# Kernel optimization log

Measured on AMD Instinct MI355X. Metric: run time of the kernel, lower is better.

The kernel has to match this reference:

```python
import jax, jax.numpy as jnp
import numpy as np

B, T, DIM, H = 4, 2048, 512, 8
DECAY = 0.9

def setup_inputs():
    key = jax.random.key(0)
    ks = jax.random.split(key, 8)
    s = 1.0 / np.sqrt(DIM)
    def lin(k):
        return jax.random.normal(k, (DIM, DIM), jnp.float32) * s
    return {
        "q": jax.random.normal(ks[0], (B, T, DIM), jnp.float32),
        "k": jax.random.normal(ks[1], (B, T, DIM), jnp.float32),
        "v": jax.random.normal(ks[2], (B, T, DIM), jnp.float32),
        "Wa": lin(ks[3]), "ba": jnp.zeros((DIM,), jnp.float32),
        "Wb": lin(ks[4]), "bb": jnp.zeros((DIM,), jnp.float32),
        "Wg": lin(ks[5]), "bg": jnp.zeros((DIM,), jnp.float32),
        "Wo": lin(ks[6]), "bo": jnp.zeros((DIM,), jnp.float32),
    }

def _linear_scan(a, b):
    # h_t = a_t * h_{t-1} + b_t along time axis=1, via associative scan
    def combine(c1, c2):
        a1, b1 = c1
        a2, b2 = c2
        return a1 * a2, a2 * b1 + b2
    return jax.lax.associative_scan(combine, (a, b), axis=1)[1]

def reference(q, k, v, Wa, ba, Wb, bb, Wg, bg, Wo, bo):
    # --- Mamba-style selective scan on q (no residual) ---
    a = jax.nn.sigmoid(q @ Wa + ba)   # input-dependent decay [B,T,D]
    b = q @ Wb + bb                   # input injection       [B,T,D]
    h = _linear_scan(a, b)            # recurrent state       [B,T,D]
    g = jax.nn.sigmoid(q @ Wg + bg)   # gate
    m_out = (h * g) @ Wo + bo         # [B,T,D]

    # --- RetNet-style decay-weighted linear retention ---
    Dh = DIM // H
    qh = q.reshape(B, T, H, Dh)
    kh = k.reshape(B, T, H, Dh)
    vh = v.reshape(B, T, H, Dh)
    t = jnp.arange(T)
    delta = t[:, None] - t[None, :]           # t - s
    mask = delta >= 0                         # causal
    decay_mat = jnp.where(
        mask,
        jnp.exp(jnp.where(mask, delta, 0).astype(jnp.float32) * np.float32(np.log(DECAY))),
        0.0,
    )                                          # [T,T]
    scores = jnp.einsum('bthd,bshd->bhts', qh, kh) * decay_mat  # [B,H,T,T]
    r_out = jnp.einsum('bhts,bshd->bthd', scores, vh).reshape(B, T, DIM)

    return m_out + r_out
```

## Files before the change

### kernel.cpp

```cpp
#include <hip/hip_runtime.h>
#include <hip/hip_bf16.h>

typedef unsigned short u16;

#define BB 4
#define TT 2048
#define DIM 512
#define NH 8
#define DH 64
#define DECAY 0.9f

#define CC 64
#define NC 32
#define BHN 32

#define CHS 32
#define NSC 64

#define TM 128
#define TN 128
#define BK 64

#define SS 72

typedef __attribute__((ext_vector_type(8))) short bf16x8;
typedef __attribute__((ext_vector_type(4))) float f32x4;

__device__ __forceinline__ u16 f2bfu(float f) {
  union { float f; unsigned int u; } c; c.f = f;
  unsigned int u = c.u + 0x7FFFu + ((c.u >> 16) & 1u);
  return (u16)(u >> 16);
}
__device__ __forceinline__ float bf2f(u16 u) {
  union { unsigned int u; float f; } c; c.u = ((unsigned int)u) << 16;
  return c.f;
}

__device__ __forceinline__ void gl_lds16(const void* g, void* l) {
  __builtin_amdgcn_global_load_lds(
      (const __attribute__((address_space(1))) void*)g,
      (__attribute__((address_space(3))) void*)(unsigned int)(unsigned long long)l,
      16, 0, 0);
}

__device__ __forceinline__ void gemm_tile(
    int nTile, int mTile, const u16* __restrict__ A, const u16* __restrict__ Bt,
    const float* __restrict__ b0, const float* __restrict__ b1,
    const float* __restrict__ b2,
    void* __restrict__ C0, void* __restrict__ C1, void* __restrict__ C2,
    int act_mask, int bf16_mask, const u16* __restrict__ Radd,
    u16* As, u16* Bs, int tid) {
  int wave = tid >> 6, lane = tid & 63;
  int group = (nTile * TN) >> 9;
  const float* bias = (group == 0) ? b0 : (group == 1) ? b1 : b2;
  void* C = (group == 0) ? C0 : (group == 1) ? C1 : C2;
  int act = (act_mask >> group) & 1;
  int isbf = (bf16_mask >> group) & 1;

  int wm = (wave >> 1) * 64, wn = (wave & 1) * 64;
  int rowA = lane & 15, khalf = lane >> 4;

  f32x4 acc[4][4];
#pragma unroll
  for (int i = 0; i < 4; ++i)
#pragma unroll
    for (int j = 0; j < 4; ++j) acc[i][j] = (f32x4){0.f, 0.f, 0.f, 0.f};

  const u16* Abase = A + (size_t)mTile * TM * 512;
  const u16* Bbase = Bt + (size_t)nTile * TN * 512;

  for (int kk = 0; kk < 512; kk += BK) {
#pragma unroll
    for (int i = 0; i < 4; ++i) {
      int o = (wave * 4 + i) * 64 + lane;
      int row = o >> 3, gk = (o & 7) ^ (row & 7);
      gl_lds16(Abase + (size_t)row * 512 + kk + gk * 8, &As[o * 8]);
    }
#pragma unroll
    for (int i = 0; i < 4; ++i) {
      int o = (wave * 4 + i) * 64 + lane;
      int row = o >> 3, gk = (o & 7) ^ (row & 7);
      gl_lds16(Bbase + (size_t)row * 512 + kk + gk * 8, &Bs[o * 8]);
    }
    __syncthreads();
#pragma unroll
    for (int k0 = 0; k0 < 2; ++k0) {
      bf16x8 af[4], bfr[4];
#pragma unroll
      for (int mi = 0; mi < 4; ++mi) {
        int rr = wm + mi * 16 + rowA;
        int gk = k0 * 4 + khalf;
        int o = rr * 8 + (gk ^ (rr & 7));
        af[mi] = *(const bf16x8*)&As[o * 8];
      }
#pragma unroll
      for (int ni = 0; ni < 4; ++ni) {
        int rr = wn + ni * 16 + rowA;
        int gk = k0 * 4 + khalf;
        int o = rr * 8 + (gk ^ (rr & 7));
        bfr[ni] = *(const bf16x8*)&Bs[o * 8];
      }
#pragma unroll
      for (int mi = 0; mi < 4; ++mi)
#pragma unroll
        for (int ni = 0; ni < 4; ++ni)
          acc[mi][ni] = __builtin_amdgcn_mfma_f32_16x16x32_bf16(
              af[mi], bfr[ni], acc[mi][ni], 0, 0, 0);
    }
    __syncthreads();
  }
  int cloc = lane & 15, rq = (lane >> 4) * 4;
#pragma unroll
  for (int mi = 0; mi < 4; ++mi) {
#pragma unroll
    for (int r = 0; r < 4; ++r) {
      int m = mTile * TM + wm + mi * 16 + rq + r;
#pragma unroll
      for (int ni = 0; ni < 4; ++ni) {
        int n = (nTile * TN + wn + ni * 16 + cloc) & 511;
        float vv = acc[mi][ni][r] + bias[n];
        if (act) vv = 1.0f / (1.0f + __expf(-vv));
        if (Radd) vv += bf2f(Radd[(size_t)m * 512 + n]);
        if (isbf) ((u16*)C)[(size_t)m * 512 + n] = f2bfu(vv);
        else ((float*)C)[(size_t)m * 512 + n] = vv;
      }
    }
  }
}

__global__ __launch_bounds__(256) void k1_prep(
    const float* __restrict__ q, u16* __restrict__ qbf,
    const float* __restrict__ W0, const float* __restrict__ W1,
    const float* __restrict__ W2, const float* __restrict__ W3,
    u16* __restrict__ Wt) {
  __shared__ float t[32][33];
  int bx = blockIdx.x, tid = threadIdx.x;
  if (bx < 1024) {
    int m = bx >> 8, rem = bx & 255;
    int n0 = (rem & 15) * 32, k0 = (rem >> 4) * 32;
    const float* W = (m == 0) ? W0 : (m == 1) ? W1 : (m == 2) ? W2 : W3;
    int tx = tid & 31, ty = tid >> 5;
#pragma unroll
    for (int r = 0; r < 32; r += 8)
      t[ty + r][tx] = W[(size_t)(k0 + ty + r) * DIM + n0 + tx];
    __syncthreads();
    u16* o = Wt + (size_t)m * DIM * DIM;
#pragma unroll
    for (int r = 0; r < 32; r += 8)
      o[(size_t)(n0 + ty + r) * DIM + k0 + tx] = f2bfu(t[tx][ty + r]);
  } else {
    int i = (bx - 1024) * 256 + tid;
    float4 f = ((const float4*)q)[i];
    ushort4 u;
    u.x = f2bfu(f.x); u.y = f2bfu(f.y); u.z = f2bfu(f.z); u.w = f2bfu(f.w);
    ((ushort4*)qbf)[i] = u;
  }
}

__global__ __launch_bounds__(256) void k2_gemm1_retkv(
    const u16* __restrict__ qbf, const u16* __restrict__ WtAll,
    const float* __restrict__ ba, const float* __restrict__ bb,
    const float* __restrict__ bg,
    float* __restrict__ Abuf, u16* __restrict__ Bb16, u16* __restrict__ Gb16,
    const float* __restrict__ k, const float* __restrict__ v,
    u16* __restrict__ KVTb, u16* __restrict__ VTg) {
  __shared__ __align__(16) u16 smem[TM * BK + TN * BK];
  int bx = blockIdx.x, tid = threadIdx.x;
  if (bx < 768) {
    gemm_tile(bx % 12, bx / 12, qbf, WtAll, ba, bb, bg, Abuf, Bb16, Gb16,
              0b101, 0b110, nullptr, smem, smem + TM * BK, tid);
    return;
  }
  int idx = bx - 768;
  int bh = idx & 31, c = idx >> 5;
  int b = bh >> 3, h = bh & 7;
  int wave = tid >> 6, lane = tid & 63;
  u16* VT = smem;
  u16* KT = smem + 64 * SS;
  size_t base = ((size_t)(b * TT + c * CC)) * DIM + h * DH;
  int row = tid >> 2, part = tid & 3, e0 = part * 16;
  float w = __powf(DECAY, (float)(63 - row));
  {
    const float4* vs = (const float4*)(v + base + (size_t)row * DIM + e0);
    const float4* ks = (const float4*)(k + base + (size_t)row * DIM + e0);
#pragma unroll
    for (int u4 = 0; u4 < 4; ++u4) {
      float4 fv = vs[u4], fk = ks[u4];
      VT[(e0 + u4 * 4 + 0) * SS + row] = f2bfu(fv.x);
      VT[(e0 + u4 * 4 + 1) * SS + row] = f2bfu(fv.y);
      VT[(e0 + u4 * 4 + 2) * SS + row] = f2bfu(fv.z);
      VT[(e0 + u4 * 4 + 3) * SS + row] = f2bfu(fv.w);
      KT[(e0 + u4 * 4 + 0) * SS + row] = f2bfu(fk.x * w);
      KT[(e0 + u4 * 4 + 1) * SS + row] = f2bfu(fk.y * w);
      KT[(e0 + u4 * 4 + 2) * SS + row] = f2bfu(fk.z * w);
      KT[(e0 + u4 * 4 + 3) * SS + row] = f2bfu(fk.w * w);
    }
  }
  __syncthreads();
  {
    int e = row;
    u16* dst = VTg + ((size_t)bh * 64 + e) * TT + c * 64 + part * 16;
    *(uint4*)dst = *(const uint4*)&VT[e * SS + part * 16];
    *(uint4*)(dst + 8) = *(const uint4*)&VT[e * SS + part * 16 + 8];
  }
  int wm = (wave >> 1) * 32, wn = (wave & 1) * 32;
  int rowA = lane & 15, khalf = lane >> 4;
  f32x4 acc[2][2];
#pragma unroll
  for (int i = 0; i < 2; ++i)
#pragma unroll
    for (int j = 0; j < 2; ++j) acc[i][j] = (f32x4){0.f, 0.f, 0.f, 0.f};
#pragma unroll
  for (int k0 = 0; k0 < 2; ++k0) {
    int gk = k0 * 4 + khalf;
    bf16x8 af[2], bfr[2];
#pragma unroll
    for (int mi = 0; mi < 2; ++mi)
      af[mi] = *(const bf16x8*)&VT[(wm + mi * 16 + rowA) * SS + gk * 8];
#pragma unroll
    for (int ni = 0; ni < 2; ++ni)
      bfr[ni] = *(const bf16x8*)&KT[(wn + ni * 16 + rowA) * SS + gk * 8];
#pragma unroll
    for (int mi = 0; mi < 2; ++mi)
#pragma unroll
      for (int ni = 0; ni < 2; ++ni)
        acc[mi][ni] = __builtin_amdgcn_mfma_f32_16x16x32_bf16(
            af[mi], bfr[ni], acc[mi][ni], 0, 0, 0);
  }
  int cloc = lane & 15, rq = (lane >> 4) * 4;
  u16* o = KVTb + ((size_t)(c * BHN + bh)) * 4096;
#pragma unroll
  for (int mi = 0; mi < 2; ++mi)
#pragma unroll
    for (int r = 0; r < 4; ++r) {
      int e = wm + mi * 16 + rq + r;
#pragma unroll
      for (int ni = 0; ni < 2; ++ni)
        o[e * 64 + (wn + ni * 16 + cloc)] = f2bfu(acc[mi][ni][r]);
    }
}

__global__ __launch_bounds__(256) void k3_part_retscan(
    const float* __restrict__ a, const u16* __restrict__ bb16,
    float* __restrict__ SA, float* __restrict__ SB,
    const u16* __restrict__ KVTb, u16* __restrict__ Ptb) {
  int bx = blockIdx.x, tid = threadIdx.x;
  if (bx < 512) {
    int ci = bx >> 3, grp = bx & 7;
    int ch = grp * 256 + tid;
    int bb = ch >> 9, d = ch & 511;
    size_t base = ((size_t)bb * TT + ci * CHS) * DIM + d;
    float h = 0.f, pA = 1.f;
#pragma unroll
    for (int t = 0; t < CHS; ++t) {
      float av = a[base + (size_t)t * DIM];
      float bv = bf2f(bb16[base + (size_t)t * DIM]);
      h = fmaf(av, h, bv);
      pA *= av;
    }
    SA[ci * 2048 + ch] = pA;
    SB[ci * 2048 + ch] = h;
  } else {
    int gid = (bx - 512) * 256 + tid;
    int bh = gid >> 12, ed = gid & 4095;
    float carry = 0.f;
    const float dC = __powf(DECAY, (float)CC);
    for (int c = 0; c < NC; ++c) {
      size_t idx = ((size_t)(c * BHN + bh)) * 4096 + ed;
      Ptb[idx] = f2bfu(carry);
      carry = fmaf(dC, carry, bf2f(KVTb[idx]));
    }
  }
}

__global__ __launch_bounds__(256) void k4_apply_retout(
    const float* __restrict__ a, const u16* __restrict__ bb16,
    const u16* __restrict__ g, const float* __restrict__ SA,
    const float* __restrict__ SB, u16* __restrict__ hg,
    const u16* __restrict__ qbf, const float* __restrict__ kg,
    const u16* __restrict__ VTg, const u16* __restrict__ Ptb,
    u16* __restrict__ routb) {
  __shared__ __align__(16) u16 Sa[64 * SS];
  __shared__ float dp[66];
  int bx = blockIdx.x, tid = threadIdx.x;
  if (bx < 512) {
    int ci = bx >> 3, grp = bx & 7;
    int ch = grp * 256 + tid;
    int bb = ch >> 9, d = ch & 511;
    float carry = 0.f;
    for (int p = 0; p < ci; ++p)
      carry = fmaf(SA[p * 2048 + ch], carry, SB[p * 2048 + ch]);
    size_t base = ((size_t)bb * TT + ci * CHS) * DIM + d;
    float h = carry;
#pragma unroll
    for (int t = 0; t < CHS; ++t) {
      size_t idx = base + (size_t)t * DIM;
      h = fmaf(a[idx], h, bf2f(bb16[idx]));
      hg[idx] = f2bfu(h * bf2f(g[idx]));
    }
    return;
  }
  int idx2 = bx - 512;
  int bh = idx2 & 31, c = idx2 >> 5;
  int b = bh >> 3, h = bh & 7;
  int wave = tid >> 6, lane = tid & 63;
  size_t base = ((size_t)(b * TT + c * CC)) * DIM + h * DH;
  if (tid < 66) dp[tid] = __powf(DECAY, (float)tid);

  int wm = (wave >> 1) * 32, wn = (wave & 1) * 32;
  int rowA = lane & 15, khalf = lane >> 4;

  bf16x8 afq[2][2];
#pragma unroll
  for (int k0 = 0; k0 < 2; ++k0)
#pragma unroll
    for (int mi = 0; mi < 2; ++mi)
      afq[k0][mi] = *(const bf16x8*)(qbf + base +
          (size_t)(wm + mi * 16 + rowA) * 512 + (k0 * 4 + khalf) * 8);
  bf16x8 bfk[2][2];
#pragma unroll
  for (int k0 = 0; k0 < 2; ++k0)
#pragma unroll
    for (int ni = 0; ni < 2; ++ni) {
      const float* kp = kg + base + (size_t)(wn + ni * 16 + rowA) * 512 +
                        (k0 * 4 + khalf) * 8;
      float4 f0 = *(const float4*)kp;
      float4 f1 = *(const float4*)(kp + 4);
      bf16x8 t;
      t[0] = (short)f2bfu(f0.x); t[1] = (short)f2bfu(f0.y);
      t[2] = (short)f2bfu(f0.z); t[3] = (short)f2bfu(f0.w);
      t[4] = (short)f2bfu(f1.x); t[5] = (short)f2bfu(f1.y);
      t[6] = (short)f2bfu(f1.z); t[7] = (short)f2bfu(f1.w);
      bfk[k0][ni] = t;
    }

  f32x4 accS[2][2];
#pragma unroll
  for (int i = 0; i < 2; ++i)
#pragma unroll
    for (int j = 0; j < 2; ++j) accS[i][j] = (f32x4){0.f, 0.f, 0.f, 0.f};
#pragma unroll
  for (int k0 = 0; k0 < 2; ++k0)
#pragma unroll
    for (int mi = 0; mi < 2; ++mi)
#pragma unroll
      for (int ni = 0; ni < 2; ++ni)
        accS[mi][ni] = __builtin_amdgcn_mfma_f32_16x16x32_bf16(
            afq[k0][mi], bfk[k0][ni], accS[mi][ni], 0, 0, 0);
  __syncthreads();

  int cloc = lane & 15, rq = (lane >> 4) * 4;
#pragma unroll
  for (int mi = 0; mi < 2; ++mi)
#pragma unroll
    for (int ni = 0; ni < 2; ++ni)
#pragma unroll
      for (int r = 0; r < 4; ++r) {
        int i = wm + mi * 16 + rq + r;
        int j = wn + ni * 16 + cloc;
        float sv = (j <= i) ? accS[mi][ni][r] * dp[i - j] : 0.f;
        Sa[i * SS + j] = f2bfu(sv);
      }
#pragma unroll
  for (int mi = 0; mi < 2; ++mi) {
    float s = dp[wm + mi * 16 + rowA + 1];
#pragma unroll
    for (int k0 = 0; k0 < 2; ++k0) {
      bf16x8 t = afq[k0][mi];
#pragma unroll
      for (int u = 0; u < 8; ++u)
        t[u] = (short)f2bfu(bf2f((u16)t[u]) * s);
      afq[k0][mi] = t;
    }
  }
  __syncthreads();

  f32x4 accO[2][2];
#pragma unroll
  for (int i = 0; i < 2; ++i)
#pragma unroll
    for (int j = 0; j < 2; ++j) accO[i][j] = (f32x4){0.f, 0.f, 0.f, 0.f};
#pragma unroll
  for (int k0 = 0; k0 < 4; ++k0) {
    bf16x8 af[2], bfv[2];
#pragma unroll
    for (int mi = 0; mi < 2; ++mi) {
      if (k0 < 2)
        af[mi] = *(const bf16x8*)&Sa[(wm + mi * 16 + rowA) * SS +
                                     (k0 * 4 + khalf) * 8];
      else
        af[mi] = afq[k0 - 2][mi];
    }
#pragma unroll
    for (int ni = 0; ni < 2; ++ni) {
      int e = wn + ni * 16 + rowA;
      if (k0 < 2)
        bfv[ni] = *(const bf16x8*)(VTg + ((size_t)bh * 64 + e) * TT + c * 64 +
                                   (k0 * 4 + khalf) * 8);
      else
        bfv[ni] = *(const bf16x8*)(Ptb + ((size_t)(c * BHN + bh)) * 4096 +
                                   e * 64 + ((k0 - 2) * 4 + khalf) * 8);
    }
#pragma unroll
    for (int mi = 0; mi < 2; ++mi)
#pragma unroll
      for (int ni = 0; ni < 2; ++ni)
        accO[mi][ni] = __builtin_amdgcn_mfma_f32_16x16x32_bf16(
            af[mi], bfv[ni], accO[mi][ni], 0, 0, 0);
  }
#pragma unroll
  for (int mi = 0; mi < 2; ++mi)
#pragma unroll
    for (int r = 0; r < 4; ++r) {
      int i = wm + mi * 16 + rq + r;
#pragma unroll
      for (int ni = 0; ni < 2; ++ni) {
        int e = wn + ni * 16 + cloc;
        routb[base + (size_t)i * 512 + e] = f2bfu(accO[mi][ni][r]);
      }
    }
}

__global__ __launch_bounds__(256) void k5_gemm2(
    const u16* __restrict__ hgbf, const u16* __restrict__ Wto,
    const float* __restrict__ bo, float* __restrict__ out,
    const u16* __restrict__ routb) {
  __shared__ __align__(16) u16 smem[TM * BK + TN * BK];
  gemm_tile(blockIdx.x, blockIdx.y, hgbf, Wto, bo, bo, bo, out, out, out,
            0, 0, routb, smem, smem + TM * BK, threadIdx.x);
}

extern "C" void kernel_launch(void* const* d_in, const int* in_sizes, int n_in,
                              void* d_out, int out_size, void* d_ws, size_t ws_size,
                              hipStream_t stream) {
  const float* q  = (const float*)d_in[0];
  const float* k  = (const float*)d_in[1];
  const float* v  = (const float*)d_in[2];
  const float* Wa = (const float*)d_in[3];
  const float* ba = (const float*)d_in[4];
  const float* Wb = (const float*)d_in[5];
  const float* bb = (const float*)d_in[6];
  const float* Wg = (const float*)d_in[7];
  const float* bg = (const float*)d_in[8];
  const float* Wo = (const float*)d_in[9];
  const float* bo = (const float*)d_in[10];
  float* out = (float*)d_out;
  float* ws = (float*)d_ws;

  const size_t NEL = (size_t)BB * TT * DIM;
  float* Abuf = ws;
  float* SA = ws + NEL;
  float* SB = SA + NSC * 2048;
  u16* up = (u16*)(SB + NSC * 2048);
  u16* Bb16  = up;  up += NEL;
  u16* Gb16  = up;  up += NEL;
  u16* qbf   = up;  up += NEL;
  u16* hgbf  = up;  up += NEL;
  u16* WtAll = up;  up += 4 * DIM * DIM;
  u16* KVTb  = up;  up += (size_t)NC * BHN * 4096;
  u16* Ptb   = up;  up += (size_t)NC * BHN * 4096;
  u16* VTg   = up;  up += (size_t)BHN * 64 * TT;
  u16* routb = up;  up += NEL;

  k1_prep<<<5120, 256, 0, stream>>>(q, qbf, Wa, Wb, Wg, Wo, WtAll);

  k2_gemm1_retkv<<<1792, 256, 0, stream>>>(qbf, WtAll, ba, bb, bg,
                                           Abuf, Bb16, Gb16, k, v, KVTb, VTg);

  k3_part_retscan<<<1024, 256, 0, stream>>>(Abuf, Bb16, SA, SB, KVTb, Ptb);

  k4_apply_retout<<<1536, 256, 0, stream>>>(Abuf, Bb16, Gb16, SA, SB, hgbf,
                                            qbf, k, VTg, Ptb, routb);

  k5_gemm2<<<dim3(4, 64), 256, 0, stream>>>(hgbf, WtAll + 3 * DIM * DIM,
                                            bo, out, routb);
}
```

Before: 198.0 us.

## Rebalance GEMM work across kernels, store decay in bf16, use 128x64 tiles

The gate projection GEMM tiles move from the first GEMM kernel into the partial-scan kernel, so they run alongside the scan and retention carry work instead of lengthening the first kernel. The sigmoid decay buffer is now stored in bf16 instead of fp32, which halves its write and read traffic across three kernels. The output GEMM switches to a 128x64 tile, giving 512 blocks instead of 256 to better fill the CUs. Storing the decay in bf16 reduces the precision of the recurrence factor, which may raise error over long scans.

```diff
diff --git a/kernel.cpp b/kernel.cpp
--- a/kernel.cpp
+++ b/kernel.cpp
@@ -47,15 +47,13 @@
     int nTile, int mTile, const u16* __restrict__ A, const u16* __restrict__ Bt,
     const float* __restrict__ b0, const float* __restrict__ b1,
     const float* __restrict__ b2,
-    void* __restrict__ C0, void* __restrict__ C1, void* __restrict__ C2,
-    int act_mask, int bf16_mask, const u16* __restrict__ Radd,
-    u16* As, u16* Bs, int tid) {
+    u16* __restrict__ C0, u16* __restrict__ C1, u16* __restrict__ C2,
+    int act_mask, u16* As, u16* Bs, int tid) {
   int wave = tid >> 6, lane = tid & 63;
   int group = (nTile * TN) >> 9;
   const float* bias = (group == 0) ? b0 : (group == 1) ? b1 : b2;
-  void* C = (group == 0) ? C0 : (group == 1) ? C1 : C2;
+  u16* C = (group == 0) ? C0 : (group == 1) ? C1 : C2;
   int act = (act_mask >> group) & 1;
-  int isbf = (bf16_mask >> group) & 1;
 
   int wm = (wave >> 1) * 64, wn = (wave & 1) * 64;
   int rowA = lane & 15, khalf = lane >> 4;
@@ -120,9 +118,80 @@
         int n = (nTile * TN + wn + ni * 16 + cloc) & 511;
         float vv = acc[mi][ni][r] + bias[n];
         if (act) vv = 1.0f / (1.0f + __expf(-vv));
-        if (Radd) vv += bf2f(Radd[(size_t)m * 512 + n]);
-        if (isbf) ((u16*)C)[(size_t)m * 512 + n] = f2bfu(vv);
-        else ((float*)C)[(size_t)m * 512 + n] = vv;
+        C[(size_t)m * 512 + n] = f2bfu(vv);
+      }
+    }
+  }
+}
+
+__device__ __forceinline__ void gemm_tile64(
+    int nTile, int mTile, const u16* __restrict__ A, const u16* __restrict__ Bt,
+    const float* __restrict__ bias, float* __restrict__ C,
+    const u16* __restrict__ Radd, u16* As, u16* Bs, int tid) {
+  int wave = tid >> 6, lane = tid & 63;
+  int wm = wave * 32;
+  int rowA = lane & 15, khalf = lane >> 4;
+
+  f32x4 acc[2][4];
+#pragma unroll
+  for (int i = 0; i < 2; ++i)
+#pragma unroll
+    for (int j = 0; j < 4; ++j) acc[i][j] = (f32x4){0.f, 0.f, 0.f, 0.f};
+
+  const u16* Abase = A + (size_t)mTile * TM * 512;
+  const u16* Bbase = Bt + (size_t)nTile * 64 * 512;
+
+  for (int kk = 0; kk < 512; kk += BK) {
+#pragma unroll
+    for (int i = 0; i < 4; ++i) {
+      int o = (wave * 4 + i) * 64 + lane;
+      int row = o >> 3, gk = (o & 7) ^ (row & 7);
+      gl_lds16(Abase + (size_t)row * 512 + kk + gk * 8, &As[o * 8]);
+    }
+#pragma unroll
+    for (int i = 0; i < 2; ++i) {
+      int o = (wave * 2 + i) * 64 + lane;
+      int row = o >> 3, gk = (o & 7) ^ (row & 7);
+      gl_lds16(Bbase + (size_t)row * 512 + kk + gk * 8, &Bs[o * 8]);
+    }
+    __syncthreads();
+#pragma unroll
+    for (int k0 = 0; k0 < 2; ++k0) {
+      bf16x8 af[2], bfr[4];
+#pragma unroll
+      for (int mi = 0; mi < 2; ++mi) {
+        int rr = wm + mi * 16 + rowA;
+        int gk = k0 * 4 + khalf;
+        int o = rr * 8 + (gk ^ (rr & 7));
+        af[mi] = *(const bf16x8*)&As[o * 8];
+      }
+#pragma unroll
+      for (int ni = 0; ni < 4; ++ni) {
+        int rr = ni * 16 + rowA;
+        int gk = k0 * 4 + khalf;
+        int o = rr * 8 + (gk ^ (rr & 7));
+        bfr[ni] = *(const bf16x8*)&Bs[o * 8];
+      }
+#pragma unroll
+      for (int mi = 0; mi < 2; ++mi)
+#pragma unroll
+        for (int ni = 0; ni < 4; ++ni)
+          acc[mi][ni] = __builtin_amdgcn_mfma_f32_16x16x32_bf16(
+              af[mi], bfr[ni], acc[mi][ni], 0, 0, 0);
+    }
+    __syncthreads();
+  }
+  int cloc = lane & 15, rq = (lane >> 4) * 4;
+#pragma unroll
+  for (int mi = 0; mi < 2; ++mi) {
+#pragma unroll
+    for (int r = 0; r < 4; ++r) {
+      int m = mTile * TM + wm + mi * 16 + rq + r;
+#pragma unroll
+      for (int ni = 0; ni < 4; ++ni) {
+        int n = nTile * 64 + ni * 16 + cloc;
+        float vv = acc[mi][ni][r] + bias[n] + bf2f(Radd[(size_t)m * 512 + n]);
+        C[(size_t)m * 512 + n] = vv;
       }
     }
   }
@@ -157,21 +226,21 @@
   }
 }
 
-__global__ __launch_bounds__(256) void k2_gemm1_retkv(
+__global__ __launch_bounds__(256) void k2_gemmab_retkv(
     const u16* __restrict__ qbf, const u16* __restrict__ WtAll,
     const float* __restrict__ ba, const float* __restrict__ bb,
     const float* __restrict__ bg,
-    float* __restrict__ Abuf, u16* __restrict__ Bb16, u16* __restrict__ Gb16,
+    u16* __restrict__ Ab16, u16* __restrict__ Bb16, u16* __restrict__ Gb16,
     const float* __restrict__ k, const float* __restrict__ v,
     u16* __restrict__ KVTb, u16* __restrict__ VTg) {
   __shared__ __align__(16) u16 smem[TM * BK + TN * BK];
   int bx = blockIdx.x, tid = threadIdx.x;
-  if (bx < 768) {
-    gemm_tile(bx % 12, bx / 12, qbf, WtAll, ba, bb, bg, Abuf, Bb16, Gb16,
-              0b101, 0b110, nullptr, smem, smem + TM * BK, tid);
+  if (bx < 512) {
+    gemm_tile(bx & 7, bx >> 3, qbf, WtAll, ba, bb, bg, Ab16, Bb16, Gb16,
+              0b101, smem, smem + TM * BK, tid);
     return;
   }
-  int idx = bx - 768;
+  int idx = bx - 512;
   int bh = idx & 31, c = idx >> 5;
   int b = bh >> 3, h = bh & 7;
   int wave = tid >> 6, lane = tid & 63;
@@ -240,28 +309,36 @@
     }
 }
 
-__global__ __launch_bounds__(256) void k3_part_retscan(
-    const float* __restrict__ a, const u16* __restrict__ bb16,
+__global__ __launch_bounds__(256) void k3_gemmg_part_retscan(
+    const u16* __restrict__ qbf, const u16* __restrict__ WtAll,
+    const float* __restrict__ ba, const float* __restrict__ bb,
+    const float* __restrict__ bg,
+    u16* __restrict__ Ab16, u16* __restrict__ Bb16, u16* __restrict__ Gb16,
     float* __restrict__ SA, float* __restrict__ SB,
     const u16* __restrict__ KVTb, u16* __restrict__ Ptb) {
+  __shared__ __align__(16) u16 smem[TM * BK + TN * BK];
   int bx = blockIdx.x, tid = threadIdx.x;
-  if (bx < 512) {
-    int ci = bx >> 3, grp = bx & 7;
+  if (bx < 256) {
+    gemm_tile(8 + (bx & 3), bx >> 2, qbf, WtAll, ba, bb, bg, Ab16, Bb16, Gb16,
+              0b101, smem, smem + TM * BK, tid);
+  } else if (bx < 768) {
+    int bxx = bx - 256;
+    int ci = bxx >> 3, grp = bxx & 7;
     int ch = grp * 256 + tid;
-    int bb = ch >> 9, d = ch & 511;
-    size_t base = ((size_t)bb * TT + ci * CHS) * DIM + d;
+    int bb2 = ch >> 9, d = ch & 511;
+    size_t base = ((size_t)bb2 * TT + ci * CHS) * DIM + d;
     float h = 0.f, pA = 1.f;
 #pragma unroll
     for (int t = 0; t < CHS; ++t) {
-      float av = a[base + (size_t)t * DIM];
-      float bv = bf2f(bb16[base + (size_t)t * DIM]);
+      float av = bf2f(Ab16[base + (size_t)t * DIM]);
+      float bv = bf2f(Bb16[base + (size_t)t * DIM]);
       h = fmaf(av, h, bv);
       pA *= av;
     }
     SA[ci * 2048 + ch] = pA;
     SB[ci * 2048 + ch] = h;
   } else {
-    int gid = (bx - 512) * 256 + tid;
+    int gid = (bx - 768) * 256 + tid;
     int bh = gid >> 12, ed = gid & 4095;
     float carry = 0.f;
     const float dC = __powf(DECAY, (float)CC);
@@ -274,7 +351,7 @@
 }
 
 __global__ __launch_bounds__(256) void k4_apply_retout(
-    const float* __restrict__ a, const u16* __restrict__ bb16,
+    const u16* __restrict__ Ab16, const u16* __restrict__ Bb16,
     const u16* __restrict__ g, const float* __restrict__ SA,
     const float* __restrict__ SB, u16* __restrict__ hg,
     const u16* __restrict__ qbf, const float* __restrict__ kg,
@@ -295,7 +372,7 @@
 #pragma unroll
     for (int t = 0; t < CHS; ++t) {
       size_t idx = base + (size_t)t * DIM;
-      h = fmaf(a[idx], h, bf2f(bb16[idx]));
+      h = fmaf(bf2f(Ab16[idx]), h, bf2f(Bb16[idx]));
       hg[idx] = f2bfu(h * bf2f(g[idx]));
     }
     return;
@@ -425,9 +502,9 @@
     const u16* __restrict__ hgbf, const u16* __restrict__ Wto,
     const float* __restrict__ bo, float* __restrict__ out,
     const u16* __restrict__ routb) {
-  __shared__ __align__(16) u16 smem[TM * BK + TN * BK];
-  gemm_tile(blockIdx.x, blockIdx.y, hgbf, Wto, bo, bo, bo, out, out, out,
-            0, 0, routb, smem, smem + TM * BK, threadIdx.x);
+  __shared__ __align__(16) u16 smem[TM * BK + 64 * BK];
+  gemm_tile64(blockIdx.x & 7, blockIdx.x >> 3, hgbf, Wto, bo, out, routb,
+              smem, smem + TM * BK, threadIdx.x);
 }
 
 extern "C" void kernel_launch(void* const* d_in, const int* in_sizes, int n_in,
@@ -448,10 +525,10 @@
   float* ws = (float*)d_ws;
 
   const size_t NEL = (size_t)BB * TT * DIM;
-  float* Abuf = ws;
-  float* SA = ws + NEL;
+  float* SA = ws;
   float* SB = SA + NSC * 2048;
   u16* up = (u16*)(SB + NSC * 2048);
+  u16* Ab16  = up;  up += NEL;
   u16* Bb16  = up;  up += NEL;
   u16* Gb16  = up;  up += NEL;
   u16* qbf   = up;  up += NEL;
@@ -464,14 +541,16 @@
 
   k1_prep<<<5120, 256, 0, stream>>>(q, qbf, Wa, Wb, Wg, Wo, WtAll);
 
-  k2_gemm1_retkv<<<1792, 256, 0, stream>>>(qbf, WtAll, ba, bb, bg,
-                                           Abuf, Bb16, Gb16, k, v, KVTb, VTg);
-
-  k3_part_retscan<<<1024, 256, 0, stream>>>(Abuf, Bb16, SA, SB, KVTb, Ptb);
-
-  k4_apply_retout<<<1536, 256, 0, stream>>>(Abuf, Bb16, Gb16, SA, SB, hgbf,
+  k2_gemmab_retkv<<<1536, 256, 0, stream>>>(qbf, WtAll, ba, bb, bg,
+                                            Ab16, Bb16, Gb16, k, v, KVTb, VTg);
+
+  k3_gemmg_part_retscan<<<1280, 256, 0, stream>>>(qbf, WtAll, ba, bb, bg,
+                                                  Ab16, Bb16, Gb16,
+                                                  SA, SB, KVTb, Ptb);
+
+  k4_apply_retout<<<1536, 256, 0, stream>>>(Ab16, Bb16, Gb16, SA, SB, hgbf,
                                             qbf, k, VTg, Ptb, routb);
 
-  k5_gemm2<<<dim3(4, 64), 256, 0, stream>>>(hgbf, WtAll + 3 * DIM * DIM,
-                                            bo, out, routb);
-}
+  k5_gemm2<<<512, 256, 0, stream>>>(hgbf, WtAll + 3 * DIM * DIM,
+                                    bo, out, routb);
+}
```

Measured after the change: 185.4 us. -6.3%, faster.

## Shrink GEMM tile to 128x64, store decay in bf16, move gate GEMM into scan kernel

Applied to the files above, without the earlier changes.

The GEMM tile is narrowed from 128x128 to 128x64, giving more blocks per launch for better CU fill, and k5 becomes a 1D grid. The sigmoid decay output is now stored as bf16 instead of fp32, cutting memory traffic for the scan passes. The gate projection GEMM moves from k2 into k3, where it runs alongside the partial scan and retention state scan, balancing work across kernels. Storing the decay in bf16 adds rounding error to the recurrence, and the narrower tile lowers data reuse per block.

```diff
diff --git a/kernel.cpp b/kernel.cpp
--- a/kernel.cpp
+++ b/kernel.cpp
@@ -18,7 +18,7 @@
 #define NSC 64
 
 #define TM 128
-#define TN 128
+#define TN 64
 #define BK 64
 
 #define SS 72
@@ -43,7 +43,7 @@
       16, 0, 0);
 }
 
-__device__ __forceinline__ void gemm_tile(
+__device__ __forceinline__ void gemm_tile64(
     int nTile, int mTile, const u16* __restrict__ A, const u16* __restrict__ Bt,
     const float* __restrict__ b0, const float* __restrict__ b1,
     const float* __restrict__ b2,
@@ -57,12 +57,12 @@
   int act = (act_mask >> group) & 1;
   int isbf = (bf16_mask >> group) & 1;
 
-  int wm = (wave >> 1) * 64, wn = (wave & 1) * 64;
+  int wm = wave * 32;
   int rowA = lane & 15, khalf = lane >> 4;
 
-  f32x4 acc[4][4];
-#pragma unroll
-  for (int i = 0; i < 4; ++i)
+  f32x4 acc[2][4];
+#pragma unroll
+  for (int i = 0; i < 2; ++i)
 #pragma unroll
     for (int j = 0; j < 4; ++j) acc[i][j] = (f32x4){0.f, 0.f, 0.f, 0.f};
 
@@ -77,17 +77,17 @@
       gl_lds16(Abase + (size_t)row * 512 + kk + gk * 8, &As[o * 8]);
     }
 #pragma unroll
-    for (int i = 0; i < 4; ++i) {
-      int o = (wave * 4 + i) * 64 + lane;
+    for (int i = 0; i < 2; ++i) {
+      int o = (wave * 2 + i) * 64 + lane;
       int row = o >> 3, gk = (o & 7) ^ (row & 7);
       gl_lds16(Bbase + (size_t)row * 512 + kk + gk * 8, &Bs[o * 8]);
     }
     __syncthreads();
 #pragma unroll
     for (int k0 = 0; k0 < 2; ++k0) {
-      bf16x8 af[4], bfr[4];
-#pragma unroll
-      for (int mi = 0; mi < 4; ++mi) {
+      bf16x8 af[2], bfr[4];
+#pragma unroll
+      for (int mi = 0; mi < 2; ++mi) {
         int rr = wm + mi * 16 + rowA;
         int gk = k0 * 4 + khalf;
         int o = rr * 8 + (gk ^ (rr & 7));
@@ -95,13 +95,13 @@
       }
 #pragma unroll
       for (int ni = 0; ni < 4; ++ni) {
-        int rr = wn + ni * 16 + rowA;
+        int rr = ni * 16 + rowA;
         int gk = k0 * 4 + khalf;
         int o = rr * 8 + (gk ^ (rr & 7));
         bfr[ni] = *(const bf16x8*)&Bs[o * 8];
       }
 #pragma unroll
-      for (int mi = 0; mi < 4; ++mi)
+      for (int mi = 0; mi < 2; ++mi)
 #pragma unroll
         for (int ni = 0; ni < 4; ++ni)
           acc[mi][ni] = __builtin_amdgcn_mfma_f32_16x16x32_bf16(
@@ -111,13 +111,13 @@
   }
   int cloc = lane & 15, rq = (lane >> 4) * 4;
 #pragma unroll
-  for (int mi = 0; mi < 4; ++mi) {
+  for (int mi = 0; mi < 2; ++mi) {
 #pragma unroll
     for (int r = 0; r < 4; ++r) {
       int m = mTile * TM + wm + mi * 16 + rq + r;
 #pragma unroll
       for (int ni = 0; ni < 4; ++ni) {
-        int n = (nTile * TN + wn + ni * 16 + cloc) & 511;
+        int n = (nTile * TN + ni * 16 + cloc) & 511;
         float vv = acc[mi][ni][r] + bias[n];
         if (act) vv = 1.0f / (1.0f + __expf(-vv));
         if (Radd) vv += bf2f(Radd[(size_t)m * 512 + n]);
@@ -157,21 +157,21 @@
   }
 }
 
-__global__ __launch_bounds__(256) void k2_gemm1_retkv(
+__global__ __launch_bounds__(256) void k2_gemmab_retkv(
     const u16* __restrict__ qbf, const u16* __restrict__ WtAll,
     const float* __restrict__ ba, const float* __restrict__ bb,
     const float* __restrict__ bg,
-    float* __restrict__ Abuf, u16* __restrict__ Bb16, u16* __restrict__ Gb16,
+    u16* __restrict__ Ab16, u16* __restrict__ Bb16, u16* __restrict__ Gb16,
     const float* __restrict__ k, const float* __restrict__ v,
     u16* __restrict__ KVTb, u16* __restrict__ VTg) {
   __shared__ __align__(16) u16 smem[TM * BK + TN * BK];
   int bx = blockIdx.x, tid = threadIdx.x;
-  if (bx < 768) {
-    gemm_tile(bx % 12, bx / 12, qbf, WtAll, ba, bb, bg, Abuf, Bb16, Gb16,
-              0b101, 0b110, nullptr, smem, smem + TM * BK, tid);
+  if (bx < 1024) {
+    gemm_tile64(bx & 15, bx >> 4, qbf, WtAll, ba, bb, bg, Ab16, Bb16, Gb16,
+                0b101, 0b111, nullptr, smem, smem + TM * BK, tid);
     return;
   }
-  int idx = bx - 768;
+  int idx = bx - 1024;
   int bh = idx & 31, c = idx >> 5;
   int b = bh >> 3, h = bh & 7;
   int wave = tid >> 6, lane = tid & 63;
@@ -240,28 +240,37 @@
     }
 }
 
-__global__ __launch_bounds__(256) void k3_part_retscan(
-    const float* __restrict__ a, const u16* __restrict__ bb16,
+__global__ __launch_bounds__(256) void k3_gemmg_part_retscan(
+    const u16* __restrict__ qbf, const u16* __restrict__ WtAll,
+    const float* __restrict__ ba, const float* __restrict__ bb,
+    const float* __restrict__ bg,
+    u16* __restrict__ Ab16, u16* __restrict__ Bb16, u16* __restrict__ Gb16,
     float* __restrict__ SA, float* __restrict__ SB,
     const u16* __restrict__ KVTb, u16* __restrict__ Ptb) {
+  __shared__ __align__(16) u16 smem[TM * BK + TN * BK];
   int bx = blockIdx.x, tid = threadIdx.x;
   if (bx < 512) {
-    int ci = bx >> 3, grp = bx & 7;
+    gemm_tile64(16 + (bx & 7), bx >> 3, qbf, WtAll, ba, bb, bg,
+                Ab16, Bb16, Gb16, 0b101, 0b111, nullptr,
+                smem, smem + TM * BK, tid);
+  } else if (bx < 1024) {
+    int bxx = bx - 512;
+    int ci = bxx >> 3, grp = bxx & 7;
     int ch = grp * 256 + tid;
-    int bb = ch >> 9, d = ch & 511;
-    size_t base = ((size_t)bb * TT + ci * CHS) * DIM + d;
+    int bb2 = ch >> 9, d = ch & 511;
+    size_t base = ((size_t)bb2 * TT + ci * CHS) * DIM + d;
     float h = 0.f, pA = 1.f;
 #pragma unroll
     for (int t = 0; t < CHS; ++t) {
-      float av = a[base + (size_t)t * DIM];
-      float bv = bf2f(bb16[base + (size_t)t * DIM]);
+      float av = bf2f(Ab16[base + (size_t)t * DIM]);
+      float bv = bf2f(Bb16[base + (size_t)t * DIM]);
       h = fmaf(av, h, bv);
       pA *= av;
     }
     SA[ci * 2048 + ch] = pA;
     SB[ci * 2048 + ch] = h;
   } else {
-    int gid = (bx - 512) * 256 + tid;
+    int gid = (bx - 1024) * 256 + tid;
     int bh = gid >> 12, ed = gid & 4095;
     float carry = 0.f;
     const float dC = __powf(DECAY, (float)CC);
@@ -274,7 +283,7 @@
 }
 
 __global__ __launch_bounds__(256) void k4_apply_retout(
-    const float* __restrict__ a, const u16* __restrict__ bb16,
+    const u16* __restrict__ Ab16, const u16* __restrict__ Bb16,
     const u16* __restrict__ g, const float* __restrict__ SA,
     const float* __restrict__ SB, u16* __restrict__ hg,
     const u16* __restrict__ qbf, const float* __restrict__ kg,
@@ -295,7 +304,7 @@
 #pragma unroll
     for (int t = 0; t < CHS; ++t) {
       size_t idx = base + (size_t)t * DIM;
-      h = fmaf(a[idx], h, bf2f(bb16[idx]));
+      h = fmaf(bf2f(Ab16[idx]), h, bf2f(Bb16[idx]));
       hg[idx] = f2bfu(h * bf2f(g[idx]));
     }
     return;
@@ -426,8 +435,8 @@
     const float* __restrict__ bo, float* __restrict__ out,
     const u16* __restrict__ routb) {
   __shared__ __align__(16) u16 smem[TM * BK + TN * BK];
-  gemm_tile(blockIdx.x, blockIdx.y, hgbf, Wto, bo, bo, bo, out, out, out,
-            0, 0, routb, smem, smem + TM * BK, threadIdx.x);
+  gemm_tile64(blockIdx.x & 7, blockIdx.x >> 3, hgbf, Wto, bo, bo, bo,
+              out, out, out, 0, 0, routb, smem, smem + TM * BK, threadIdx.x);
 }
 
 extern "C" void kernel_launch(void* const* d_in, const int* in_sizes, int n_in,
@@ -448,10 +457,10 @@
   float* ws = (float*)d_ws;
 
   const size_t NEL = (size_t)BB * TT * DIM;
-  float* Abuf = ws;
-  float* SA = ws + NEL;
+  float* SA = ws;
   float* SB = SA + NSC * 2048;
   u16* up = (u16*)(SB + NSC * 2048);
+  u16* Ab16  = up;  up += NEL;
   u16* Bb16  = up;  up += NEL;
   u16* Gb16  = up;  up += NEL;
   u16* qbf   = up;  up += NEL;
@@ -464,14 +473,16 @@
 
   k1_prep<<<5120, 256, 0, stream>>>(q, qbf, Wa, Wb, Wg, Wo, WtAll);
 
-  k2_gemm1_retkv<<<1792, 256, 0, stream>>>(qbf, WtAll, ba, bb, bg,
-                                           Abuf, Bb16, Gb16, k, v, KVTb, VTg);
-
-  k3_part_retscan<<<1024, 256, 0, stream>>>(Abuf, Bb16, SA, SB, KVTb, Ptb);
-
-  k4_apply_retout<<<1536, 256, 0, stream>>>(Abuf, Bb16, Gb16, SA, SB, hgbf,
+  k2_gemmab_retkv<<<2048, 256, 0, stream>>>(qbf, WtAll, ba, bb, bg,
+                                            Ab16, Bb16, Gb16, k, v, KVTb, VTg);
+
+  k3_gemmg_part_retscan<<<1536, 256, 0, stream>>>(qbf, WtAll, ba, bb, bg,
+                                                  Ab16, Bb16, Gb16,
+                                                  SA, SB, KVTb, Ptb);
+
+  k4_apply_retout<<<1536, 256, 0, stream>>>(Ab16, Bb16, Gb16, SA, SB, hgbf,
                                             qbf, k, VTg, Ptb, routb);
 
-  k5_gemm2<<<dim3(4, 64), 256, 0, stream>>>(hgbf, WtAll + 3 * DIM * DIM,
-                                            bo, out, routb);
-}
+  k5_gemm2<<<512, 256, 0, stream>>>(hgbf, WtAll + 3 * DIM * DIM,
+                                    bo, out, routb);
+}
```

Result: faster. 191.8 us (-3.1%).
